# Performance work log

Hardware: AMD Instinct MI355X
Metric: run time of the kernel (lower is better)

Reference implementation:

```python
import jax, jax.numpy as jnp
import numpy as np

B, G, N = 32, 512, 512          # batch, group (POMO rollouts), problem size
EMB, H, DK = 128, 8, 16          # embedding_dim, head_num, qkv_dim (H*DK == EMB)
E, FH, K = 8, 512, 2             # num_experts, ff_hidden_dim, top-k
SQRT_EMB = 11.313708498984761    # sqrt(128), model_params['sqrt_embedding_dim']
CLIP = 10.0                      # logit_clipping


def setup_inputs() -> dict:
    key = jax.random.key(0)
    ks = jax.random.split(key, 22)
    s = 0.05
    d = {}
    d["pref"] = jax.random.uniform(ks[0], (2,), dtype=jnp.float32)
    d["graph"] = jax.random.normal(ks[1], (B, 1, EMB), dtype=jnp.float32)
    d["capacity"] = jax.random.uniform(ks[2], (B, G), dtype=jnp.float32)
    d["encoded_nodes"] = jax.random.normal(ks[3], (B, N, EMB), dtype=jnp.float32)
    d["ninf_mask"] = jnp.zeros((B, G, N), dtype=jnp.float32)
    # hyper-network MLP (note: original has NO activations between hyper_fc layers)
    d["fc1_w"] = jax.random.normal(ks[4], (256, 2)) * s
    d["fc1_b"] = jax.random.normal(ks[5], (256,)) * s
    d["fc2_w"] = jax.random.normal(ks[6], (256, 256)) * s
    d["fc2_b"] = jax.random.normal(ks[7], (256,)) * s
    d["fc3_w"] = jax.random.normal(ks[8], (8, 256)) * s
    d["fc3_b"] = jax.random.normal(ks[9], (8,)) * s
    # hyper heads producing the attention weight matrices (Linear(embd_dim=2, out), no bias)
    d["hWq"] = jax.random.normal(ks[10], ((1 + EMB) * H * DK, 2)) * 0.02
    d["hWk"] = jax.random.normal(ks[11], (EMB * H * DK, 2)) * 0.02
    d["hWv"] = jax.random.normal(ks[12], (EMB * H * DK, 2)) * 0.02
    d["hWc"] = jax.random.normal(ks[13], (EMB * H * DK, 2)) * 0.02
    # MoE combine layer: gating (token input + 8-dim pref embedding) and E expert MLPs
    d["gate_w"] = jax.random.normal(ks[14], (H * DK, E)) * s
    d["gate_pref_w"] = jax.random.normal(ks[15], (8, E)) * s
    d["e_w1"] = jax.random.normal(ks[16], (E, FH, H * DK)) * (1.0 / np.sqrt(H * DK))
    d["e_b1"] = jnp.zeros((E, FH), dtype=jnp.float32)
    d["e_w2"] = jax.random.normal(ks[17], (E, EMB, FH)) * (1.0 / np.sqrt(FH))
    d["e_b2"] = jnp.zeros((E, EMB), dtype=jnp.float32)
    d = {k2: v.astype(jnp.float32) for k2, v in d.items()}
    return d


def _heads(x):  # [B, n, H*DK] -> [B, H, n, DK]
    b, n, _ = x.shape
    return x.reshape(b, n, H, DK).transpose(0, 2, 1, 3)


def reference(pref, graph, capacity, encoded_nodes, ninf_mask,
              fc1_w, fc1_b, fc2_w, fc2_b, fc3_w, fc3_b,
              hWq, hWk, hWv, hWc,
              gate_w, gate_pref_w, e_w1, e_b1, e_w2, e_b2):
    # ---- assign(pref): hypernet generates attention weight matrices ----
    h = fc1_w @ pref + fc1_b
    h = fc2_w @ h + fc2_b
    mid = fc3_w @ h + fc3_b                      # [8] == mid_embd_pref
    Wq = (hWq @ mid[0:2]).reshape(H * DK, 1 + EMB)
    Wk = (hWk @ mid[2:4]).reshape(H * DK, EMB)
    Wv = (hWv @ mid[4:6]).reshape(H * DK, EMB)
    Wc = (hWc @ mid[6:8]).reshape(H * DK, EMB)
    # ---- set_kv ----
    k = _heads(encoded_nodes @ Wk.T)             # [B,H,N,DK]
    v = _heads(encoded_nodes @ Wv.T)
    # ---- forward ----
    inp = jnp.concatenate(
        [jnp.broadcast_to(graph, (B, G, EMB)), capacity[:, :, None]], axis=2)
    q = _heads(inp @ Wq.T)                       # [B,H,G,DK]
    score = jnp.einsum('bhgd,bhnd->bhgn', q, k) / jnp.sqrt(jnp.float32(DK))
    score = score + ninf_mask[:, None, :, :]
    attn = jax.nn.softmax(score, axis=3)
    out = jnp.einsum('bhgn,bhnd->bhgd', attn, v)
    out = out.transpose(0, 2, 1, 3).reshape(B, G, H * DK)   # [B,G,128]
    # ---- MoE combine (noisy top-k gating, deterministic at inference) ----
    logits = out @ gate_w + mid @ gate_pref_w    # [B,G,E]
    vals, idx = jax.lax.top_k(logits, K)
    gv = jax.nn.softmax(vals, axis=-1)           # softmax over selected k (T=1)
    gates = jnp.sum(jax.nn.one_hot(idx, E, dtype=out.dtype) * gv[..., None], axis=-2)
    hdn = jax.nn.relu(jnp.einsum('bgi,ehi->bgeh', out, e_w1) + e_b1)
    y = jnp.einsum('bgeh,eoh->bgeo', hdn, e_w2) + e_b2
    moe_out = jnp.einsum('bgeo,bge->bgo', y, gates)          # [B,G,EMB]
    # ---- combine + tanh-clipped masked softmax over nodes ----
    mh = moe_out @ Wc.T                           # [B,G,EMB]
    sc = jnp.einsum('bge,bne->bgn', mh, encoded_nodes) / SQRT_EMB
    probs = jax.nn.softmax(CLIP * jnp.tanh(sc) + ninf_mask, axis=2)
    return probs
```

## Files before the change

kernel.cpp:

```cpp
#include <hip/hip_runtime.h>


typedef __attribute__((ext_vector_type(8))) __bf16 bf16x8;
typedef __attribute__((ext_vector_type(4))) float f32x4;

static constexpr long OFF_MID   = 0;
static constexpr long OFF_PREFL = 8;
static constexpr long OFF_WQ    = 64;
static constexpr long OFF_WKB   = 16576;
static constexpr long OFF_WVB   = 24768;
static constexpr long OFF_WCB   = 32960;
static constexpr long OFF_QB    = 65728;
static constexpr long OFF_CNT   = 69824;
static constexpr long OFF_TOK   = 69888;
static constexpr long OFF_WGT   = 200960;
static constexpr long OFF_AO    = 332288;
static constexpr long OFF_MH    = 2429440;
static constexpr long OFF_ENCB  = 3478016;

__device__ __forceinline__ unsigned f2bf(float x) {
  union { float f; unsigned u; } v; v.f = x;
  return ((v.u + 0x7FFFu + ((v.u >> 16) & 1u)) >> 16) & 0xFFFFu;
}

__global__ __launch_bounds__(256)
void k_hyper(const float* __restrict__ pref, const float* __restrict__ fc1w,
             const float* __restrict__ fc1b, const float* __restrict__ fc2w,
             const float* __restrict__ fc2b, const float* __restrict__ fc3w,
             const float* __restrict__ fc3b, const float* __restrict__ gpw,
             float* __restrict__ ws) {
  __shared__ float h1[256];
  __shared__ float h2[256];
  __shared__ float mid[8];
  const int t = threadIdx.x;
  const float p0 = pref[0], p1 = pref[1];
  h1[t] = fc1w[2*t]*p0 + fc1w[2*t+1]*p1 + fc1b[t];
  __syncthreads();
  float s = 0.f;
  for (int j = 0; j < 256; ++j) s = fmaf(fc2w[t*256+j], h1[j], s);
  h2[t] = s + fc2b[t];
  __syncthreads();
  if (t < 8) {
    float s2 = 0.f;
    for (int j = 0; j < 256; ++j) s2 = fmaf(fc3w[t*256+j], h2[j], s2);
    mid[t] = s2 + fc3b[t];
    ws[OFF_MID + t] = mid[t];
  }
  __syncthreads();
  if (t < 8) {
    float s3 = 0.f;
    for (int i = 0; i < 8; ++i) s3 = fmaf(mid[i], gpw[i*8 + t], s3);
    ws[OFF_PREFL + t] = s3;
  }
}

__global__ __launch_bounds__(256)
void k_hyperw(const float* __restrict__ hWq, const float* __restrict__ hWk,
              const float* __restrict__ hWv, const float* __restrict__ hWc,
              float* __restrict__ ws) {
  const int i = blockIdx.x*256 + threadIdx.x;
  const float m0 = ws[0], m1 = ws[1], m2 = ws[2], m3 = ws[3],
              m4 = ws[4], m5 = ws[5], m6 = ws[6], m7 = ws[7];
  if (i < 16512) {
    ws[OFF_WQ + i] = hWq[2*i]*m0 + hWq[2*i+1]*m1;
  } else if (i < 32896) {
    const int j = i - 16512;
    ((unsigned short*)(ws + OFF_WKB))[j] = (unsigned short)f2bf(hWk[2*j]*m2 + hWk[2*j+1]*m3);
  } else if (i < 49280) {
    const int j = i - 32896;
    ((unsigned short*)(ws + OFF_WVB))[j] = (unsigned short)f2bf(hWv[2*j]*m4 + hWv[2*j+1]*m5);
  } else if (i < 65664) {
    const int j = i - 49280;
    ((unsigned short*)(ws + OFF_WCB))[j] = (unsigned short)f2bf(hWc[2*j]*m6 + hWc[2*j+1]*m7);
  }
}

__global__ __launch_bounds__(256)
void k_cvt(const float* __restrict__ ew1, const float* __restrict__ ew2,
           const float* __restrict__ enc,
           unsigned short* __restrict__ w1b, unsigned short* __restrict__ w2b,
           unsigned short* __restrict__ encb) {
  const int i = blockIdx.x*256 + threadIdx.x;
  const float* src;
  unsigned short* dst;
  if (i < 131072)      { src = ew1 + (long)i*4;          dst = w1b + (long)i*4; }
  else if (i < 262144) { src = ew2 + (long)(i-131072)*4; dst = w2b + (long)(i-131072)*4; }
  else                 { src = enc + (long)(i-262144)*4; dst = encb + (long)(i-262144)*4; }
  const float4 v = *(const float4*)src;
  uint2 p;
  p.x = f2bf(v.x) | (f2bf(v.y) << 16);
  p.y = f2bf(v.z) | (f2bf(v.w) << 16);
  *(uint2*)dst = p;
}

__global__ __launch_bounds__(128)
void k_qbase(const float* __restrict__ graph, float* __restrict__ ws) {
  __shared__ float g[128];
  const int b = blockIdx.x, t = threadIdx.x;
  g[t] = graph[b*128 + t];
  __syncthreads();
  const float* wq = ws + OFF_WQ + (long)t*129;
  float s = 0.f;
  for (int i = 0; i < 128; ++i) s = fmaf(g[i], wq[i], s);
  ws[OFF_QB + b*128 + t] = s;
}

__device__ __forceinline__ bf16x8 ld_frag(const unsigned short* base, int row, int bytecol) {
  const int addr = row*256 + (bytecol ^ ((row & 7) << 4));
  return *(const bf16x8*)((const char*)base + addr);
}

__global__ __launch_bounds__(256)
void k_kv(const unsigned short* __restrict__ encb,
          const unsigned short* __restrict__ wkb,
          const unsigned short* __restrict__ wvb,
          unsigned short* __restrict__ Kb, unsigned short* __restrict__ Vb) {
  __shared__ unsigned short Ws[128*128];
  __shared__ unsigned short Xs[64*128];
  const int tid = threadIdx.x;
  const int nbase = blockIdx.x * 64;
  const unsigned short* Wb = blockIdx.y ? wvb : wkb;
  unsigned short* Cb = blockIdx.y ? Vb : Kb;
#pragma unroll
  for (int s = 0; s < 8; ++s) {
    const int id = tid + s*256;
    const int fr = id >> 4, c16 = id & 15;
    const uint4 v = *(const uint4*)(Wb + (long)fr*128 + c16*8);
    *(uint4*)((char*)Ws + fr*256 + ((c16*16) ^ ((fr & 7) << 4))) = v;
  }
#pragma unroll
  for (int s = 0; s < 4; ++s) {
    const int id = tid + s*256;
    const int r = id >> 4, c16 = id & 15;
    const uint4 v = *(const uint4*)(encb + (long)(nbase + r)*128 + c16*8);
    *(uint4*)((char*)Xs + r*256 + ((c16*16) ^ ((r & 7) << 4))) = v;
  }
  __syncthreads();
  const int w = tid >> 6, l = tid & 63, lq = l >> 4, lr = l & 15;
  f32x4 acc[2][4];
#pragma unroll
  for (int a = 0; a < 2; ++a)
#pragma unroll
    for (int m = 0; m < 4; ++m) acc[a][m] = (f32x4){0.f, 0.f, 0.f, 0.f};
#pragma unroll
  for (int ks = 0; ks < 4; ++ks) {
    const int bcol = ks*64 + lq*16;
    const bf16x8 a0 = ld_frag(Ws, (2*w  )*16 + lr, bcol);
    const bf16x8 a1 = ld_frag(Ws, (2*w+1)*16 + lr, bcol);
    const bf16x8 b0 = ld_frag(Xs, 0*16 + lr, bcol);
    const bf16x8 b1 = ld_frag(Xs, 1*16 + lr, bcol);
    const bf16x8 b2 = ld_frag(Xs, 2*16 + lr, bcol);
    const bf16x8 b3 = ld_frag(Xs, 3*16 + lr, bcol);
    acc[0][0] = __builtin_amdgcn_mfma_f32_16x16x32_bf16(a0, b0, acc[0][0], 0, 0, 0);
    acc[0][1] = __builtin_amdgcn_mfma_f32_16x16x32_bf16(a0, b1, acc[0][1], 0, 0, 0);
    acc[0][2] = __builtin_amdgcn_mfma_f32_16x16x32_bf16(a0, b2, acc[0][2], 0, 0, 0);
    acc[0][3] = __builtin_amdgcn_mfma_f32_16x16x32_bf16(a0, b3, acc[0][3], 0, 0, 0);
    acc[1][0] = __builtin_amdgcn_mfma_f32_16x16x32_bf16(a1, b0, acc[1][0], 0, 0, 0);
    acc[1][1] = __builtin_amdgcn_mfma_f32_16x16x32_bf16(a1, b1, acc[1][1], 0, 0, 0);
    acc[1][2] = __builtin_amdgcn_mfma_f32_16x16x32_bf16(a1, b2, acc[1][2], 0, 0, 0);
    acc[1][3] = __builtin_amdgcn_mfma_f32_16x16x32_bf16(a1, b3, acc[1][3], 0, 0, 0);
  }
#pragma unroll
  for (int obi = 0; obi < 2; ++obi) {
    const int o0 = (2*w + obi)*16 + lq*4;
#pragma unroll
    for (int mb = 0; mb < 4; ++mb) {
      const long n = nbase + mb*16 + lr;
      uint2 pp;
      pp.x = f2bf(acc[obi][mb][0]) | (f2bf(acc[obi][mb][1]) << 16);
      pp.y = f2bf(acc[obi][mb][2]) | (f2bf(acc[obi][mb][3]) << 16);
      *(uint2*)(Cb + n*128 + o0) = pp;
    }
  }
}

__global__ __launch_bounds__(256)
void k_mh(const float* __restrict__ Y0, const float* __restrict__ Y1,
          const unsigned short* __restrict__ wcb,
          unsigned short* __restrict__ mhb) {
  __shared__ unsigned short Ws[128*128];
  __shared__ unsigned short Xs[64*128];
  const int tid = threadIdx.x;
  const int nbase = blockIdx.x * 64;
#pragma unroll
  for (int s = 0; s < 8; ++s) {
    const int id = tid + s*256;
    const int fr = id >> 4, c16 = id & 15;
    const uint4 v = *(const uint4*)(wcb + (long)fr*128 + c16*8);
    *(uint4*)((char*)Ws + fr*256 + ((c16*16) ^ ((fr & 7) << 4))) = v;
  }
#pragma unroll
  for (int s = 0; s < 4; ++s) {
    const int id = tid + s*256;
    const int r = id >> 4, c16 = id & 15;
    const long base = (long)(nbase + r)*128 + c16*8;
    const float4 a0 = *(const float4*)(Y0 + base);
    const float4 a1 = *(const float4*)(Y0 + base + 4);
    const float4 b0 = *(const float4*)(Y1 + base);
    const float4 b1 = *(const float4*)(Y1 + base + 4);
    uint4 p;
    p.x = f2bf(a0.x + b0.x) | (f2bf(a0.y + b0.y) << 16);
    p.y = f2bf(a0.z + b0.z) | (f2bf(a0.w + b0.w) << 16);
    p.z = f2bf(a1.x + b1.x) | (f2bf(a1.y + b1.y) << 16);
    p.w = f2bf(a1.z + b1.z) | (f2bf(a1.w + b1.w) << 16);
    *(uint4*)((char*)Xs + r*256 + ((c16*16) ^ ((r & 7) << 4))) = p;
  }
  __syncthreads();
  const int w = tid >> 6, l = tid & 63, lq = l >> 4, lr = l & 15;
  f32x4 acc[2][4];
#pragma unroll
  for (int a = 0; a < 2; ++a)
#pragma unroll
    for (int m = 0; m < 4; ++m) acc[a][m] = (f32x4){0.f, 0.f, 0.f, 0.f};
#pragma unroll
  for (int ks = 0; ks < 4; ++ks) {
    const int bcol = ks*64 + lq*16;
    const bf16x8 a0 = ld_frag(Ws, (2*w  )*16 + lr, bcol);
    const bf16x8 a1 = ld_frag(Ws, (2*w+1)*16 + lr, bcol);
    const bf16x8 b0 = ld_frag(Xs, 0*16 + lr, bcol);
    const bf16x8 b1 = ld_frag(Xs, 1*16 + lr, bcol);
    const bf16x8 b2 = ld_frag(Xs, 2*16 + lr, bcol);
    const bf16x8 b3 = ld_frag(Xs, 3*16 + lr, bcol);
    acc[0][0] = __builtin_amdgcn_mfma_f32_16x16x32_bf16(a0, b0, acc[0][0], 0, 0, 0);
    acc[0][1] = __builtin_amdgcn_mfma_f32_16x16x32_bf16(a0, b1, acc[0][1], 0, 0, 0);
    acc[0][2] = __builtin_amdgcn_mfma_f32_16x16x32_bf16(a0, b2, acc[0][2], 0, 0, 0);
    acc[0][3] = __builtin_amdgcn_mfma_f32_16x16x32_bf16(a0, b3, acc[0][3], 0, 0, 0);
    acc[1][0] = __builtin_amdgcn_mfma_f32_16x16x32_bf16(a1, b0, acc[1][0], 0, 0, 0);
    acc[1][1] = __builtin_amdgcn_mfma_f32_16x16x32_bf16(a1, b1, acc[1][1], 0, 0, 0);
    acc[1][2] = __builtin_amdgcn_mfma_f32_16x16x32_bf16(a1, b2, acc[1][2], 0, 0, 0);
    acc[1][3] = __builtin_amdgcn_mfma_f32_16x16x32_bf16(a1, b3, acc[1][3], 0, 0, 0);
  }
#pragma unroll
  for (int obi = 0; obi < 2; ++obi) {
    const int o0 = (2*w + obi)*16 + lq*4;
#pragma unroll
    for (int mb = 0; mb < 4; ++mb) {
      const long n = nbase + mb*16 + lr;
      uint2 pp;
      pp.x = f2bf(acc[obi][mb][0]) | (f2bf(acc[obi][mb][1]) << 16);
      pp.y = f2bf(acc[obi][mb][2]) | (f2bf(acc[obi][mb][3]) << 16);
      *(uint2*)(mhb + n*128 + o0) = pp;
    }
  }
}

__global__ __launch_bounds__(512)
void k_attn(const unsigned short* __restrict__ Kb,
            const unsigned short* __restrict__ Vb,
            const float* __restrict__ ws, const float* __restrict__ cap,
            const float* __restrict__ mask, float* __restrict__ AO) {
  const int bid = blockIdx.x;
  const int b = bid & 31, h = (bid >> 5) & 7, qh = bid >> 8;
  __shared__ unsigned short Kbf[512*24];
  __shared__ unsigned short Vt[16*536];
  __shared__ unsigned short Ps[8*16*136];
  const int tid = threadIdx.x;
#pragma unroll
  for (int it = 0; it < 2; ++it) {
    const int i = tid + it*512;
    const int n = i >> 1, hf = i & 1;
    const long src = (long)(b*512 + n)*128 + h*16 + hf*8;
    const uint4 kv = *(const uint4*)(Kb + src);
    *(uint4*)(Kbf + n*24 + hf*8) = kv;
    const uint4 vv = *(const uint4*)(Vb + src);
    const unsigned short* sp = (const unsigned short*)&vv;
#pragma unroll
    for (int j = 0; j < 8; ++j) Vt[(hf*8 + j)*536 + n] = sp[j];
  }
  const int w = tid >> 6, l = tid & 63;
  const int lq = l >> 4, lr = l & 15;
  float qb8[8], wl8[8];
  if (lq < 2) {
    const float* qbp = ws + OFF_QB + b*128 + h*16 + lq*8;
    const float* wqp = ws + OFF_WQ;
#pragma unroll
    for (int j = 0; j < 8; ++j) {
      qb8[j] = qbp[j];
      wl8[j] = wqp[(h*16 + lq*8 + j)*129 + 128];
    }
  }
  unsigned short* Pw = Ps + w*16*136;
  __syncthreads();
  const float SC = 0.25f;
  for (int qb = 0; qb < 2; ++qb) {
    const int grow = qh*256 + w*32 + qb*16 + lr;
    bf16x8 qf;
    {
      union { uint4 u; bf16x8 v; } cv;
      cv.u = make_uint4(0u, 0u, 0u, 0u);
      if (lq < 2) {
        const float cp = cap[b*512 + grow];
        float qv[8];
#pragma unroll
        for (int j = 0; j < 8; ++j) qv[j] = (qb8[j] + cp*wl8[j]) * SC;
        cv.u.x = f2bf(qv[0]) | (f2bf(qv[1]) << 16);
        cv.u.y = f2bf(qv[2]) | (f2bf(qv[3]) << 16);
        cv.u.z = f2bf(qv[4]) | (f2bf(qv[5]) << 16);
        cv.u.w = f2bf(qv[6]) | (f2bf(qv[7]) << 16);
      }
      qf = cv.v;
    }
    float m = -3.0e38f, lsum = 0.f;
    f32x4 oacc = {0.f, 0.f, 0.f, 0.f};
    const float* mrow = mask + ((long)(b*512 + grow))*512 + lq*4;
    float4 mk[8];
#pragma unroll
    for (int nb = 0; nb < 8; ++nb) mk[nb] = *(const float4*)(mrow + nb*16);
    for (int ch = 0; ch < 4; ++ch) {
      const int n0 = ch*128;
      f32x4 s[8];
#pragma unroll
      for (int nb = 0; nb < 8; ++nb) {
        bf16x8 kf;
        {
          union { uint4 u; bf16x8 v; } cv;
          cv.u = make_uint4(0u, 0u, 0u, 0u);
          if (lq < 2) cv.u = *(const uint4*)(Kbf + (n0 + nb*16 + lr)*24 + lq*8);
          kf = cv.v;
        }
        s[nb] = __builtin_amdgcn_mfma_f32_16x16x32_bf16(
            kf, qf, (f32x4){0.f, 0.f, 0.f, 0.f}, 0, 0, 0);
        s[nb][0] += mk[nb].x; s[nb][1] += mk[nb].y;
        s[nb][2] += mk[nb].z; s[nb][3] += mk[nb].w;
      }
      if (ch < 3) {
#pragma unroll
        for (int nb = 0; nb < 8; ++nb)
          mk[nb] = *(const float4*)(mrow + (ch+1)*128 + nb*16);
      }
      f32x4 mx = s[0];
#pragma unroll
      for (int nb = 1; nb < 8; ++nb) {
        mx[0] = fmaxf(mx[0], s[nb][0]); mx[1] = fmaxf(mx[1], s[nb][1]);
        mx[2] = fmaxf(mx[2], s[nb][2]); mx[3] = fmaxf(mx[3], s[nb][3]);
      }
      float cm = fmaxf(fmaxf(mx[0], mx[1]), fmaxf(mx[2], mx[3]));
      cm = fmaxf(cm, __shfl_xor(cm, 16));
      cm = fmaxf(cm, __shfl_xor(cm, 32));
      const float nm = fmaxf(m, cm);
      const float rs = __expf(m - nm);
      lsum *= rs;
      oacc[0] *= rs; oacc[1] *= rs; oacc[2] *= rs; oacc[3] *= rs;
      m = nm;
      float ls = 0.f;
#pragma unroll
      for (int nb = 0; nb < 8; ++nb) {
        const float p0 = __expf(s[nb][0] - m);
        const float p1 = __expf(s[nb][1] - m);
        const float p2 = __expf(s[nb][2] - m);
        const float p3 = __expf(s[nb][3] - m);
        ls += (p0 + p1) + (p2 + p3);
        uint2 pp;
        asm("v_cvt_pk_bf16_f32 %0, %1, %2" : "=v"(pp.x) : "v"(p0), "v"(p1));
        asm("v_cvt_pk_bf16_f32 %0, %1, %2" : "=v"(pp.y) : "v"(p2), "v"(p3));
        *(uint2*)(Pw + lr*136 + nb*16 + lq*4) = pp;
      }
      lsum += ls;
#pragma unroll
      for (int ks = 0; ks < 4; ++ks) {
        const bf16x8 va = *(const bf16x8*)(Vt + lr*536 + n0 + ks*32 + lq*8);
        const bf16x8 pb = *(const bf16x8*)(Pw + lr*136 + ks*32 + lq*8);
        oacc = __builtin_amdgcn_mfma_f32_16x16x32_bf16(va, pb, oacc, 0, 0, 0);
      }
    }
    lsum += __shfl_xor(lsum, 16);
    lsum += __shfl_xor(lsum, 32);
    const float inv = 1.f / lsum;
    float4 o;
    o.x = oacc[0]*inv; o.y = oacc[1]*inv; o.z = oacc[2]*inv; o.w = oacc[3]*inv;
    *(float4*)(AO + (long)(b*512 + grow)*128 + h*16 + lq*4) = o;
  }
}

__global__ __launch_bounds__(256)
void k_gate(const float* __restrict__ AO, const float* __restrict__ gw,
            float* __restrict__ ws) {
  const int tid = threadIdx.x;
  const int t = blockIdx.x*256 + tid;
  const float* x = AO + (long)t*128;
  float lg[8];
  {
    const float* pl = ws + OFF_PREFL;
#pragma unroll
    for (int e = 0; e < 8; ++e) lg[e] = pl[e];
  }
  for (int i = 0; i < 128; i += 4) {
    const float4 xv = *(const float4*)(x + i);
#pragma unroll
    for (int u = 0; u < 4; ++u) {
      const float xi = (&xv.x)[u];
      const float4 ga = *(const float4*)(gw + (i+u)*8);
      const float4 gb = *(const float4*)(gw + (i+u)*8 + 4);
      lg[0] = fmaf(xi, ga.x, lg[0]); lg[1] = fmaf(xi, ga.y, lg[1]);
      lg[2] = fmaf(xi, ga.z, lg[2]); lg[3] = fmaf(xi, ga.w, lg[3]);
      lg[4] = fmaf(xi, gb.x, lg[4]); lg[5] = fmaf(xi, gb.y, lg[5]);
      lg[6] = fmaf(xi, gb.z, lg[6]); lg[7] = fmaf(xi, gb.w, lg[7]);
    }
  }
  int i0 = 0; float v0 = lg[0];
#pragma unroll
  for (int e = 1; e < 8; ++e) if (lg[e] > v0) { v0 = lg[e]; i0 = e; }
  int i1 = -1; float v1 = -1e30f;
#pragma unroll
  for (int e = 0; e < 8; ++e) if (e != i0 && lg[e] > v1) { v1 = lg[e]; i1 = e; }
  const float e1 = __expf(v1 - v0);
  const float w0 = 1.f / (1.f + e1);
  const float w1 = 1.f - w0;
  __shared__ int bcnt[8];
  __shared__ int gbase[8];
  if (tid < 8) bcnt[tid] = 0;
  __syncthreads();
  const int p0 = atomicAdd(&bcnt[i0], 1);
  const int p1 = atomicAdd(&bcnt[i1], 1);
  __syncthreads();
  if (tid < 8) {
    int* cnt = (int*)(ws + OFF_CNT);
    gbase[tid] = (bcnt[tid] > 0) ? atomicAdd(&cnt[tid], bcnt[tid]) : 0;
  }
  __syncthreads();
  int* tokp = (int*)(ws + OFF_TOK);
  float* wgtp = ws + OFF_WGT;
  const int s0 = gbase[i0] + p0;
  tokp[i0*16384 + s0] = t;
  wgtp[i0*16384 + s0] = w0;
  const int s1 = gbase[i1] + p1;
  tokp[i1*16384 + s1] = t | (1 << 30);
  wgtp[i1*16384 + s1] = w1;
}

__global__ __launch_bounds__(256)
void k_moe(const float* __restrict__ AO,
           const unsigned short* __restrict__ w1b,
           const unsigned short* __restrict__ w2b,
           const float* __restrict__ eb1, const float* __restrict__ eb2,
           float* __restrict__ ws,
           float* __restrict__ Y0, float* __restrict__ Y1) {
  const int e = blockIdx.y;
  const int ce = ((const int*)(ws + OFF_CNT))[e];
  const int base = blockIdx.x * 64;
  if (base >= ce) return;
  const int nt = min(64, ce - base);

  __shared__ unsigned short Xs[64*128];
  __shared__ unsigned short Wts[128*128];
  __shared__ unsigned short Hs[64*128];
  __shared__ float seb1[512];
  __shared__ float seb2[128];
  __shared__ int   stok[64];
  __shared__ float swgt[64];

  const int tid = threadIdx.x;
  if (tid < 64) {
    if (tid < nt) {
      stok[tid] = ((const int*)(ws + OFF_TOK))[e*16384 + base + tid];
      swgt[tid] = (ws + OFF_WGT)[e*16384 + base + tid];
    } else { stok[tid] = -1; swgt[tid] = 0.f; }
  }
  for (int i = tid; i < 512; i += 256) seb1[i] = eb1[e*512 + i];
  if (tid < 128) seb2[tid] = eb2[e*128 + tid];
  __syncthreads();

#pragma unroll
  for (int r8 = 0; r8 < 8; ++r8) {
    const int id = tid + r8*256;
    const int r = id >> 5, c = id & 31;
    const int pk = stok[r];
    float4 xv = make_float4(0.f, 0.f, 0.f, 0.f);
    if (pk >= 0) xv = *(const float4*)(AO + (long)(pk & 0x3FFFFFFF)*128 + c*4);
    uint2 pkd;
    pkd.x = f2bf(xv.x) | (f2bf(xv.y) << 16);
    pkd.y = f2bf(xv.z) | (f2bf(xv.w) << 16);
    const int bc = (c*8) ^ ((r & 7) << 4);
    *(uint2*)((char*)Xs + r*256 + bc) = pkd;
  }

  const int w  = tid >> 6;
  const int l  = tid & 63;
  const int lq = l >> 4;
  const int lr = l & 15;

  f32x4 yacc[2][4];
#pragma unroll
  for (int a = 0; a < 2; ++a)
#pragma unroll
    for (int m = 0; m < 4; ++m) yacc[a][m] = (f32x4){0.f, 0.f, 0.f, 0.f};

  for (int fc = 0; fc < 4; ++fc) {
    __syncthreads();
    {
      const long wb = (long)(e*512 + fc*128) * 128;
#pragma unroll
      for (int s = 0; s < 8; ++s) {
        const int id = tid + s*256;
        const int fr = id >> 4, c16 = id & 15;
        const uint4 v = *(const uint4*)(w1b + wb + (long)fr*128 + c16*8);
        *(uint4*)((char*)Wts + fr*256 + ((c16*16) ^ ((fr & 7) << 4))) = v;
      }
    }
    __syncthreads();
    f32x4 hacc[2][4];
#pragma unroll
    for (int a = 0; a < 2; ++a)
#pragma unroll
      for (int m = 0; m < 4; ++m) hacc[a][m] = (f32x4){0.f, 0.f, 0.f, 0.f};
#pragma unroll
    for (int ks = 0; ks < 4; ++ks) {
      const int bcol = ks*64 + lq*16;
      const bf16x8 a0 = ld_frag(Wts, (2*w  )*16 + lr, bcol);
      const bf16x8 a1 = ld_frag(Wts, (2*w+1)*16 + lr, bcol);
      const bf16x8 b0 = ld_frag(Xs,  0*16 + lr, bcol);
      const bf16x8 b1 = ld_frag(Xs,  1*16 + lr, bcol);
      const bf16x8 b2 = ld_frag(Xs,  2*16 + lr, bcol);
      const bf16x8 b3 = ld_frag(Xs,  3*16 + lr, bcol);
      hacc[0][0] = __builtin_amdgcn_mfma_f32_16x16x32_bf16(a0, b0, hacc[0][0], 0, 0, 0);
      hacc[0][1] = __builtin_amdgcn_mfma_f32_16x16x32_bf16(a0, b1, hacc[0][1], 0, 0, 0);
      hacc[0][2] = __builtin_amdgcn_mfma_f32_16x16x32_bf16(a0, b2, hacc[0][2], 0, 0, 0);
      hacc[0][3] = __builtin_amdgcn_mfma_f32_16x16x32_bf16(a0, b3, hacc[0][3], 0, 0, 0);
      hacc[1][0] = __builtin_amdgcn_mfma_f32_16x16x32_bf16(a1, b0, hacc[1][0], 0, 0, 0);
      hacc[1][1] = __builtin_amdgcn_mfma_f32_16x16x32_bf16(a1, b1, hacc[1][1], 0, 0, 0);
      hacc[1][2] = __builtin_amdgcn_mfma_f32_16x16x32_bf16(a1, b2, hacc[1][2], 0, 0, 0);
      hacc[1][3] = __builtin_amdgcn_mfma_f32_16x16x32_bf16(a1, b3, hacc[1][3], 0, 0, 0);
    }
    __syncthreads();
#pragma unroll
    for (int fbi = 0; fbi < 2; ++fbi) {
      const int fb = (2*w + fbi)*16 + lq*4;
      const float4 bia = *(const float4*)&seb1[fc*128 + fb];
#pragma unroll
      for (int mb = 0; mb < 4; ++mb) {
        const int m = mb*16 + lr;
        const float h0 = fmaxf(hacc[fbi][mb][0] + bia.x, 0.f);
        const float h1 = fmaxf(hacc[fbi][mb][1] + bia.y, 0.f);
        const float h2 = fmaxf(hacc[fbi][mb][2] + bia.z, 0.f);
        const float h3 = fmaxf(hacc[fbi][mb][3] + bia.w, 0.f);
        uint2 p;
        p.x = f2bf(h0) | (f2bf(h1) << 16);
        p.y = f2bf(h2) | (f2bf(h3) << 16);
        const int bc = (fb*2) ^ ((m & 7) << 4);
        *(uint2*)((char*)Hs + m*256 + bc) = p;
      }
    }
    {
      const long wb = (long)(e*128) * 512 + fc*128;
#pragma unroll
      for (int s = 0; s < 8; ++s) {
        const int id = tid + s*256;
        const int orr = id >> 4, c16 = id & 15;
        const uint4 v = *(const uint4*)(w2b + wb + (long)orr*512 + c16*8);
        *(uint4*)((char*)Wts + orr*256 + ((c16*16) ^ ((orr & 7) << 4))) = v;
      }
    }
    __syncthreads();
#pragma unroll
    for (int ks = 0; ks < 4; ++ks) {
      const int bcol = ks*64 + lq*16;
      const bf16x8 a0 = ld_frag(Wts, (2*w  )*16 + lr, bcol);
      const bf16x8 a1 = ld_frag(Wts, (2*w+1)*16 + lr, bcol);
      const bf16x8 b0 = ld_frag(Hs,  0*16 + lr, bcol);
      const bf16x8 b1 = ld_frag(Hs,  1*16 + lr, bcol);
      const bf16x8 b2 = ld_frag(Hs,  2*16 + lr, bcol);
      const bf16x8 b3 = ld_frag(Hs,  3*16 + lr, bcol);
      yacc[0][0] = __builtin_amdgcn_mfma_f32_16x16x32_bf16(a0, b0, yacc[0][0], 0, 0, 0);
      yacc[0][1] = __builtin_amdgcn_mfma_f32_16x16x32_bf16(a0, b1, yacc[0][1], 0, 0, 0);
      yacc[0][2] = __builtin_amdgcn_mfma_f32_16x16x32_bf16(a0, b2, yacc[0][2], 0, 0, 0);
      yacc[0][3] = __builtin_amdgcn_mfma_f32_16x16x32_bf16(a0, b3, yacc[0][3], 0, 0, 0);
      yacc[1][0] = __builtin_amdgcn_mfma_f32_16x16x32_bf16(a1, b0, yacc[1][0], 0, 0, 0);
      yacc[1][1] = __builtin_amdgcn_mfma_f32_16x16x32_bf16(a1, b1, yacc[1][1], 0, 0, 0);
      yacc[1][2] = __builtin_amdgcn_mfma_f32_16x16x32_bf16(a1, b2, yacc[1][2], 0, 0, 0);
      yacc[1][3] = __builtin_amdgcn_mfma_f32_16x16x32_bf16(a1, b3, yacc[1][3], 0, 0, 0);
    }
  }
#pragma unroll
  for (int obi = 0; obi < 2; ++obi) {
    const int ob = (2*w + obi)*16 + lq*4;
    const float4 b2 = *(const float4*)&seb2[ob];
#pragma unroll
    for (int mb = 0; mb < 4; ++mb) {
      const int tl = mb*16 + lr;
      if (tl < nt) {
        const int pk = stok[tl];
        const int tk = pk & 0x3FFFFFFF;
        const float wgt = swgt[tl];
        float* Yp = ((pk >> 30) ? Y1 : Y0) + (long)tk*128 + ob;
        float4 o;
        o.x = (yacc[obi][mb][0] + b2.x) * wgt;
        o.y = (yacc[obi][mb][1] + b2.y) * wgt;
        o.z = (yacc[obi][mb][2] + b2.z) * wgt;
        o.w = (yacc[obi][mb][3] + b2.w) * wgt;
        *(float4*)Yp = o;
      }
    }
  }
}

__global__ __launch_bounds__(512)
void k_gemm2f(const unsigned short* __restrict__ mhb,
              const unsigned short* __restrict__ encb,
              const float* __restrict__ mask,
              float* __restrict__ out) {
  const int bid = blockIdx.x;
  const int b = bid & 31, rt = bid >> 5;
  __shared__ unsigned short Amh[64*128];
  __shared__ unsigned short Bch[512*32];
  __shared__ float red[64][9];
  const int tid = threadIdx.x;
  const int w = tid >> 6, l = tid & 63, lq = l >> 4, lr = l & 15;
  const long rowbase = (long)b*512 + rt*64;
#pragma unroll
  for (int s = 0; s < 2; ++s) {
    const int id = tid + s*512;
    const int r = id >> 4, c16 = id & 15;
    const uint4 v = *(const uint4*)(mhb + (rowbase + r)*128 + c16*8);
    *(uint4*)((char*)Amh + r*256 + ((c16*16) ^ ((r & 7) << 4))) = v;
  }
  f32x4 acc[4][4];
#pragma unroll
  for (int mi = 0; mi < 4; ++mi)
#pragma unroll
    for (int ni = 0; ni < 4; ++ni) acc[mi][ni] = (f32x4){0.f, 0.f, 0.f, 0.f};
  for (int kc = 0; kc < 4; ++kc) {
    __syncthreads();
#pragma unroll
    for (int s = 0; s < 4; ++s) {
      const int id = tid + s*512;
      const int n = id >> 2, sl = id & 3;
      const uint4 v = *(const uint4*)(encb + ((long)b*512 + n)*128 + kc*32 + sl*8);
      *(uint4*)((char*)Bch + n*64 + ((sl*16) ^ ((n & 3) << 4))) = v;
    }
    __syncthreads();
    bf16x8 af[4], bfr[4];
#pragma unroll
    for (int mi = 0; mi < 4; ++mi) {
      const int r = mi*16 + lr;
      af[mi] = *(const bf16x8*)((const char*)Amh + r*256 + ((kc*64 + lq*16) ^ ((r & 7) << 4)));
    }
#pragma unroll
    for (int ni = 0; ni < 4; ++ni) {
      const int n = w*64 + ni*16 + lr;
      bfr[ni] = *(const bf16x8*)((const char*)Bch + n*64 + ((lq*16) ^ ((n & 3) << 4)));
    }
#pragma unroll
    for (int mi = 0; mi < 4; ++mi)
#pragma unroll
      for (int ni = 0; ni < 4; ++ni)
        acc[mi][ni] = __builtin_amdgcn_mfma_f32_16x16x32_bf16(af[mi], bfr[ni], acc[mi][ni], 0, 0, 0);
  }
  const float ISC = 1.f/11.313708498984761f;
  float rsum[4][4];
#pragma unroll
  for (int mi = 0; mi < 4; ++mi)
#pragma unroll
    for (int j = 0; j < 4; ++j) rsum[mi][j] = 0.f;
#pragma unroll
  for (int mi = 0; mi < 4; ++mi) {
#pragma unroll
    for (int j = 0; j < 4; ++j) {
      const long row = rowbase + mi*16 + lq*4 + j;
      const float* mrow = mask + row*512 + w*64 + lr;
#pragma unroll
      for (int ni = 0; ni < 4; ++ni) {
        const float sc = acc[mi][ni][j] * ISC;
        const float li = 10.f*tanhf(sc) + mrow[ni*16];
        const float e = __expf(li - 10.f);
        acc[mi][ni][j] = e;
        rsum[mi][j] += e;
      }
    }
  }
#pragma unroll
  for (int mi = 0; mi < 4; ++mi)
#pragma unroll
    for (int j = 0; j < 4; ++j) {
#pragma unroll
      for (int o = 1; o < 16; o <<= 1) rsum[mi][j] += __shfl_xor(rsum[mi][j], o);
    }
  if (lr == 0) {
#pragma unroll
    for (int mi = 0; mi < 4; ++mi)
#pragma unroll
      for (int j = 0; j < 4; ++j) red[mi*16 + lq*4 + j][w] = rsum[mi][j];
  }
  __syncthreads();
  if (tid < 64) {
    float s = 0.f;
#pragma unroll
    for (int wv = 0; wv < 8; ++wv) s += red[tid][wv];
    red[tid][8] = 1.f / s;
  }
  __syncthreads();
#pragma unroll
  for (int mi = 0; mi < 4; ++mi) {
#pragma unroll
    for (int j = 0; j < 4; ++j) {
      const int rl = mi*16 + lq*4 + j;
      const float inv = red[rl][8];
      float* orow = out + (rowbase + rl)*512 + w*64 + lr;
#pragma unroll
      for (int ni = 0; ni < 4; ++ni) orow[ni*16] = acc[mi][ni][j] * inv;
    }
  }
}

extern "C" void kernel_launch(void* const* d_in, const int* in_sizes, int n_in,
                              void* d_out, int out_size, void* d_ws, size_t ws_size,
                              hipStream_t stream) {
  (void)in_sizes; (void)n_in; (void)out_size; (void)ws_size;
  const float* pref  = (const float*)d_in[0];
  const float* graph = (const float*)d_in[1];
  const float* cap   = (const float*)d_in[2];
  const float* enc   = (const float*)d_in[3];
  const float* mask  = (const float*)d_in[4];
  const float* fc1w  = (const float*)d_in[5];
  const float* fc1b  = (const float*)d_in[6];
  const float* fc2w  = (const float*)d_in[7];
  const float* fc2b  = (const float*)d_in[8];
  const float* fc3w  = (const float*)d_in[9];
  const float* fc3b  = (const float*)d_in[10];
  const float* hWq   = (const float*)d_in[11];
  const float* hWk   = (const float*)d_in[12];
  const float* hWv   = (const float*)d_in[13];
  const float* hWc   = (const float*)d_in[14];
  const float* gw    = (const float*)d_in[15];
  const float* gpw   = (const float*)d_in[16];
  const float* ew1   = (const float*)d_in[17];
  const float* eb1   = (const float*)d_in[18];
  const float* ew2   = (const float*)d_in[19];
  const float* eb2   = (const float*)d_in[20];
  float* ws  = (float*)d_ws;
  float* out = (float*)d_out;
  unsigned short* Kbuf = (unsigned short*)out;
  unsigned short* Vbuf = (unsigned short*)(out + 1048576);
  float* Y0 = out;
  float* Y1 = out + 2097152;
  unsigned short* ew1b = (unsigned short*)(out + 4194304);
  unsigned short* ew2b = (unsigned short*)(out + 4456448);
  unsigned short* mhb  = (unsigned short*)(ws + OFF_MH);
  unsigned short* encb = (unsigned short*)(ws + OFF_ENCB);
  unsigned short* wkb  = (unsigned short*)(ws + OFF_WKB);
  unsigned short* wvb  = (unsigned short*)(ws + OFF_WVB);
  unsigned short* wcb  = (unsigned short*)(ws + OFF_WCB);

  hipMemsetAsync((char*)d_ws + OFF_CNT*sizeof(float), 0, 8*sizeof(int), stream);
  k_cvt<<<3072, 256, 0, stream>>>(ew1, ew2, enc, ew1b, ew2b, encb);
  k_hyper<<<1, 256, 0, stream>>>(pref, fc1w, fc1b, fc2w, fc2b, fc3w, fc3b, gpw, ws);
  k_hyperw<<<257, 256, 0, stream>>>(hWq, hWk, hWv, hWc, ws);
  k_qbase<<<32, 128, 0, stream>>>(graph, ws);
  k_kv<<<dim3(256, 2), 256, 0, stream>>>(encb, wkb, wvb, Kbuf, Vbuf);
  k_attn<<<512, 512, 0, stream>>>(Kbuf, Vbuf, ws, cap, mask, ws + OFF_AO);
  k_gate<<<64, 256, 0, stream>>>(ws + OFF_AO, gw, ws);
  k_moe<<<dim3(256, 8), 256, 0, stream>>>(ws + OFF_AO, ew1b, ew2b, eb1, eb2, ws, Y0, Y1);
  k_mh<<<256, 256, 0, stream>>>(Y0, Y1, wcb, mhb);
  k_gemm2f<<<256, 512, 0, stream>>>(mhb, encb, mask, out);
}
```

Measured before the change: 132.6 us.

## Fuse prep kernels into one launch and retile attention for more blocks

Merges the bf16 conversion, hyper-network MLP, hyper weight generation, q-base projection and counter reset into a single k_prep launch, recomputing the small MLP per block to avoid serial kernel dependencies. Restructures the attention kernel to 1024 blocks with 16 query rows per wave and 32-key chunks, replacing padded LDS layouts with XOR swizzles and setting occupancy bounds. Trades redundant MLP compute and more online-softmax rescale steps for fewer launches and higher parallelism and occupancy.

```diff
diff --git a/kernel.cpp b/kernel.cpp
--- a/kernel.cpp
+++ b/kernel.cpp
@@ -6,17 +6,17 @@
 
 static constexpr long OFF_MID   = 0;
 static constexpr long OFF_PREFL = 8;
-static constexpr long OFF_WQ    = 64;
-static constexpr long OFF_WKB   = 16576;
-static constexpr long OFF_WVB   = 24768;
-static constexpr long OFF_WCB   = 32960;
-static constexpr long OFF_QB    = 65728;
-static constexpr long OFF_CNT   = 69824;
-static constexpr long OFF_TOK   = 69888;
-static constexpr long OFF_WGT   = 200960;
-static constexpr long OFF_AO    = 332288;
-static constexpr long OFF_MH    = 2429440;
-static constexpr long OFF_ENCB  = 3478016;
+static constexpr long OFF_WL    = 16;
+static constexpr long OFF_WKB   = 256;
+static constexpr long OFF_WVB   = 8448;
+static constexpr long OFF_WCB   = 16640;
+static constexpr long OFF_QB    = 24832;
+static constexpr long OFF_CNT   = 28928;
+static constexpr long OFF_TOK   = 28936;
+static constexpr long OFF_WGT   = 160008;
+static constexpr long OFF_AO    = 291080;
+static constexpr long OFF_MH    = 2388232;
+static constexpr long OFF_ENCB  = 3436808;
 
 __device__ __forceinline__ unsigned f2bf(float x) {
   union { float f; unsigned u; } v; v.f = x;
@@ -24,85 +24,97 @@
 }
 
 __global__ __launch_bounds__(256)
-void k_hyper(const float* __restrict__ pref, const float* __restrict__ fc1w,
-             const float* __restrict__ fc1b, const float* __restrict__ fc2w,
-             const float* __restrict__ fc2b, const float* __restrict__ fc3w,
-             const float* __restrict__ fc3b, const float* __restrict__ gpw,
-             float* __restrict__ ws) {
+void k_prep(const float* __restrict__ pref, const float* __restrict__ fc1w,
+            const float* __restrict__ fc1b, const float* __restrict__ fc2w,
+            const float* __restrict__ fc2b, const float* __restrict__ fc3w,
+            const float* __restrict__ fc3b, const float* __restrict__ gpw,
+            const float* __restrict__ graph,
+            const float* __restrict__ hWq, const float* __restrict__ hWk,
+            const float* __restrict__ hWv, const float* __restrict__ hWc,
+            const float* __restrict__ ew1, const float* __restrict__ ew2,
+            const float* __restrict__ enc,
+            unsigned short* __restrict__ w1b, unsigned short* __restrict__ w2b,
+            unsigned short* __restrict__ encb, float* __restrict__ ws) {
+  const int bid = blockIdx.x;
+  const int tid = threadIdx.x;
+  if (bid < 3072) {
+    const int i = bid*256 + tid;
+    const float* src;
+    unsigned short* dst;
+    if (i < 131072)      { src = ew1 + (long)i*4;          dst = w1b + (long)i*4; }
+    else if (i < 262144) { src = ew2 + (long)(i-131072)*4; dst = w2b + (long)(i-131072)*4; }
+    else                 { src = enc + (long)(i-262144)*4; dst = encb + (long)(i-262144)*4; }
+    const float4 v = *(const float4*)src;
+    uint2 p;
+    p.x = f2bf(v.x) | (f2bf(v.y) << 16);
+    p.y = f2bf(v.z) | (f2bf(v.w) << 16);
+    *(uint2*)dst = p;
+    return;
+  }
   __shared__ float h1[256];
   __shared__ float h2[256];
   __shared__ float mid[8];
-  const int t = threadIdx.x;
+  __shared__ float g[2][128];
   const float p0 = pref[0], p1 = pref[1];
-  h1[t] = fc1w[2*t]*p0 + fc1w[2*t+1]*p1 + fc1b[t];
+  h1[tid] = fc1w[2*tid]*p0 + fc1w[2*tid+1]*p1 + fc1b[tid];
   __syncthreads();
   float s = 0.f;
-  for (int j = 0; j < 256; ++j) s = fmaf(fc2w[t*256+j], h1[j], s);
-  h2[t] = s + fc2b[t];
-  __syncthreads();
-  if (t < 8) {
+  for (int j = 0; j < 256; ++j) s = fmaf(fc2w[tid*256+j], h1[j], s);
+  h2[tid] = s + fc2b[tid];
+  __syncthreads();
+  if (tid < 8) {
     float s2 = 0.f;
-    for (int j = 0; j < 256; ++j) s2 = fmaf(fc3w[t*256+j], h2[j], s2);
-    mid[t] = s2 + fc3b[t];
-    ws[OFF_MID + t] = mid[t];
-  }
-  __syncthreads();
-  if (t < 8) {
-    float s3 = 0.f;
-    for (int i = 0; i < 8; ++i) s3 = fmaf(mid[i], gpw[i*8 + t], s3);
-    ws[OFF_PREFL + t] = s3;
-  }
-}
-
-__global__ __launch_bounds__(256)
-void k_hyperw(const float* __restrict__ hWq, const float* __restrict__ hWk,
-              const float* __restrict__ hWv, const float* __restrict__ hWc,
-              float* __restrict__ ws) {
-  const int i = blockIdx.x*256 + threadIdx.x;
-  const float m0 = ws[0], m1 = ws[1], m2 = ws[2], m3 = ws[3],
-              m4 = ws[4], m5 = ws[5], m6 = ws[6], m7 = ws[7];
-  if (i < 16512) {
-    ws[OFF_WQ + i] = hWq[2*i]*m0 + hWq[2*i+1]*m1;
-  } else if (i < 32896) {
-    const int j = i - 16512;
-    ((unsigned short*)(ws + OFF_WKB))[j] = (unsigned short)f2bf(hWk[2*j]*m2 + hWk[2*j+1]*m3);
-  } else if (i < 49280) {
-    const int j = i - 32896;
-    ((unsigned short*)(ws + OFF_WVB))[j] = (unsigned short)f2bf(hWv[2*j]*m4 + hWv[2*j+1]*m5);
-  } else if (i < 65664) {
-    const int j = i - 49280;
-    ((unsigned short*)(ws + OFF_WCB))[j] = (unsigned short)f2bf(hWc[2*j]*m6 + hWc[2*j+1]*m7);
-  }
-}
-
-__global__ __launch_bounds__(256)
-void k_cvt(const float* __restrict__ ew1, const float* __restrict__ ew2,
-           const float* __restrict__ enc,
-           unsigned short* __restrict__ w1b, unsigned short* __restrict__ w2b,
-           unsigned short* __restrict__ encb) {
-  const int i = blockIdx.x*256 + threadIdx.x;
-  const float* src;
-  unsigned short* dst;
-  if (i < 131072)      { src = ew1 + (long)i*4;          dst = w1b + (long)i*4; }
-  else if (i < 262144) { src = ew2 + (long)(i-131072)*4; dst = w2b + (long)(i-131072)*4; }
-  else                 { src = enc + (long)(i-262144)*4; dst = encb + (long)(i-262144)*4; }
-  const float4 v = *(const float4*)src;
-  uint2 p;
-  p.x = f2bf(v.x) | (f2bf(v.y) << 16);
-  p.y = f2bf(v.z) | (f2bf(v.w) << 16);
-  *(uint2*)dst = p;
-}
-
-__global__ __launch_bounds__(128)
-void k_qbase(const float* __restrict__ graph, float* __restrict__ ws) {
-  __shared__ float g[128];
-  const int b = blockIdx.x, t = threadIdx.x;
-  g[t] = graph[b*128 + t];
-  __syncthreads();
-  const float* wq = ws + OFF_WQ + (long)t*129;
-  float s = 0.f;
-  for (int i = 0; i < 128; ++i) s = fmaf(g[i], wq[i], s);
-  ws[OFF_QB + b*128 + t] = s;
+    for (int j = 0; j < 256; ++j) s2 = fmaf(fc3w[tid*256+j], h2[j], s2);
+    mid[tid] = s2 + fc3b[tid];
+  }
+  __syncthreads();
+  if (bid < 3264) {
+    const int i = (bid - 3072)*256 + tid;
+    if (i < 16384) {
+      ((unsigned short*)(ws + OFF_WKB))[i] =
+          (unsigned short)f2bf(hWk[2*i]*mid[2] + hWk[2*i+1]*mid[3]);
+    } else if (i < 32768) {
+      const int j = i - 16384;
+      ((unsigned short*)(ws + OFF_WVB))[j] =
+          (unsigned short)f2bf(hWv[2*j]*mid[4] + hWv[2*j+1]*mid[5]);
+    } else {
+      const int j = i - 32768;
+      ((unsigned short*)(ws + OFF_WCB))[j] =
+          (unsigned short)f2bf(hWc[2*j]*mid[6] + hWc[2*j+1]*mid[7]);
+    }
+    return;
+  }
+  const int qb = bid - 3264;
+  const int b0 = qb*2;
+  {
+    const int bb = tid >> 7, ii = tid & 127;
+    g[bb][ii] = graph[(b0+bb)*128 + ii];
+  }
+  __syncthreads();
+  const float m0 = mid[0], m1 = mid[1];
+  {
+    const int bb = tid >> 7, o = tid & 127;
+    const float* hq = hWq + (long)o*129*2;
+    float acc = 0.f;
+    for (int i2 = 0; i2 < 128; ++i2) {
+      const float w = hq[2*i2]*m0 + hq[2*i2+1]*m1;
+      acc = fmaf(g[bb][i2], w, acc);
+    }
+    ws[OFF_QB + (b0+bb)*128 + o] = acc;
+  }
+  if (qb == 0) {
+    if (tid < 8) {
+      ws[OFF_MID + tid] = mid[tid];
+      float s3 = 0.f;
+      for (int i2 = 0; i2 < 8; ++i2) s3 = fmaf(mid[i2], gpw[i2*8 + tid], s3);
+      ws[OFF_PREFL + tid] = s3;
+      ((int*)(ws + OFF_CNT))[tid] = 0;
+    }
+    if (tid >= 16 && tid < 144) {
+      const int o = tid - 16;
+      ws[OFF_WL + o] = hWq[((long)o*129 + 128)*2]*m0 + hWq[((long)o*129 + 128)*2 + 1]*m1;
+    }
+  }
 }
 
 __device__ __forceinline__ bf16x8 ld_frag(const unsigned short* base, int row, int bytecol) {
@@ -244,16 +256,16 @@
   }
 }
 
-__global__ __launch_bounds__(512)
+__global__ __launch_bounds__(512, 8)
 void k_attn(const unsigned short* __restrict__ Kb,
             const unsigned short* __restrict__ Vb,
             const float* __restrict__ ws, const float* __restrict__ cap,
             const float* __restrict__ mask, float* __restrict__ AO) {
   const int bid = blockIdx.x;
   const int b = bid & 31, h = (bid >> 5) & 7, qh = bid >> 8;
-  __shared__ unsigned short Kbf[512*24];
-  __shared__ unsigned short Vt[16*536];
-  __shared__ unsigned short Ps[8*16*136];
+  __shared__ unsigned short Kbf[512*16];
+  __shared__ unsigned short Vt[16*512];
+  __shared__ unsigned short Ps[8*16*32];
   const int tid = threadIdx.x;
 #pragma unroll
   for (int it = 0; it < 2; ++it) {
@@ -261,115 +273,94 @@
     const int n = i >> 1, hf = i & 1;
     const long src = (long)(b*512 + n)*128 + h*16 + hf*8;
     const uint4 kv = *(const uint4*)(Kb + src);
-    *(uint4*)(Kbf + n*24 + hf*8) = kv;
+    *(uint4*)(Kbf + n*16 + hf*8) = kv;
     const uint4 vv = *(const uint4*)(Vb + src);
     const unsigned short* sp = (const unsigned short*)&vv;
 #pragma unroll
-    for (int j = 0; j < 8; ++j) Vt[(hf*8 + j)*536 + n] = sp[j];
+    for (int j = 0; j < 8; ++j) {
+      const int d = hf*8 + j;
+      Vt[d*512 + (n ^ ((d & 7) << 3))] = sp[j];
+    }
   }
   const int w = tid >> 6, l = tid & 63;
   const int lq = l >> 4, lr = l & 15;
-  float qb8[8], wl8[8];
-  if (lq < 2) {
-    const float* qbp = ws + OFF_QB + b*128 + h*16 + lq*8;
-    const float* wqp = ws + OFF_WQ;
-#pragma unroll
-    for (int j = 0; j < 8; ++j) {
-      qb8[j] = qbp[j];
-      wl8[j] = wqp[(h*16 + lq*8 + j)*129 + 128];
-    }
-  }
-  unsigned short* Pw = Ps + w*16*136;
-  __syncthreads();
-  const float SC = 0.25f;
-  for (int qb = 0; qb < 2; ++qb) {
-    const int grow = qh*256 + w*32 + qb*16 + lr;
-    bf16x8 qf;
-    {
-      union { uint4 u; bf16x8 v; } cv;
-      cv.u = make_uint4(0u, 0u, 0u, 0u);
-      if (lq < 2) {
-        const float cp = cap[b*512 + grow];
-        float qv[8];
-#pragma unroll
-        for (int j = 0; j < 8; ++j) qv[j] = (qb8[j] + cp*wl8[j]) * SC;
-        cv.u.x = f2bf(qv[0]) | (f2bf(qv[1]) << 16);
-        cv.u.y = f2bf(qv[2]) | (f2bf(qv[3]) << 16);
-        cv.u.z = f2bf(qv[4]) | (f2bf(qv[5]) << 16);
-        cv.u.w = f2bf(qv[6]) | (f2bf(qv[7]) << 16);
+  const int grow = qh*128 + w*16 + lr;
+  bf16x8 qf;
+  {
+    union { uint4 u; bf16x8 v; } cv;
+    cv.u = make_uint4(0u, 0u, 0u, 0u);
+    if (lq < 2) {
+      const float* qbp = ws + OFF_QB + b*128 + h*16 + lq*8;
+      const float* wlp = ws + OFF_WL + h*16 + lq*8;
+      const float cp = cap[b*512 + grow];
+      float qv[8];
+#pragma unroll
+      for (int j = 0; j < 8; ++j) qv[j] = (qbp[j] + cp*wlp[j]) * 0.25f;
+      cv.u.x = f2bf(qv[0]) | (f2bf(qv[1]) << 16);
+      cv.u.y = f2bf(qv[2]) | (f2bf(qv[3]) << 16);
+      cv.u.z = f2bf(qv[4]) | (f2bf(qv[5]) << 16);
+      cv.u.w = f2bf(qv[6]) | (f2bf(qv[7]) << 16);
+    }
+    qf = cv.v;
+  }
+  unsigned short* Pw = Ps + w*16*32;
+  const int psw = (lr & 3) << 3;
+  __syncthreads();
+  float m = -3.0e38f, lsum = 0.f;
+  f32x4 oacc = {0.f, 0.f, 0.f, 0.f};
+  const float* mrow = mask + ((long)(b*512 + grow))*512 + lq*4;
+  for (int qc = 0; qc < 16; ++qc) {
+    const int n0 = qc*32;
+    f32x4 s[2];
+#pragma unroll
+    for (int nb = 0; nb < 2; ++nb) {
+      bf16x8 kf;
+      {
+        union { uint4 u; bf16x8 v; } cv;
+        cv.u = make_uint4(0u, 0u, 0u, 0u);
+        if (lq < 2) cv.u = *(const uint4*)(Kbf + (n0 + nb*16 + lr)*16 + lq*8);
+        kf = cv.v;
       }
-      qf = cv.v;
-    }
-    float m = -3.0e38f, lsum = 0.f;
-    f32x4 oacc = {0.f, 0.f, 0.f, 0.f};
-    const float* mrow = mask + ((long)(b*512 + grow))*512 + lq*4;
-    float4 mk[8];
-#pragma unroll
-    for (int nb = 0; nb < 8; ++nb) mk[nb] = *(const float4*)(mrow + nb*16);
-    for (int ch = 0; ch < 4; ++ch) {
-      const int n0 = ch*128;
-      f32x4 s[8];
-#pragma unroll
-      for (int nb = 0; nb < 8; ++nb) {
-        bf16x8 kf;
-        {
-          union { uint4 u; bf16x8 v; } cv;
-          cv.u = make_uint4(0u, 0u, 0u, 0u);
-          if (lq < 2) cv.u = *(const uint4*)(Kbf + (n0 + nb*16 + lr)*24 + lq*8);
-          kf = cv.v;
-        }
-        s[nb] = __builtin_amdgcn_mfma_f32_16x16x32_bf16(
-            kf, qf, (f32x4){0.f, 0.f, 0.f, 0.f}, 0, 0, 0);
-        s[nb][0] += mk[nb].x; s[nb][1] += mk[nb].y;
-        s[nb][2] += mk[nb].z; s[nb][3] += mk[nb].w;
-      }
-      if (ch < 3) {
-#pragma unroll
-        for (int nb = 0; nb < 8; ++nb)
-          mk[nb] = *(const float4*)(mrow + (ch+1)*128 + nb*16);
-      }
-      f32x4 mx = s[0];
-#pragma unroll
-      for (int nb = 1; nb < 8; ++nb) {
-        mx[0] = fmaxf(mx[0], s[nb][0]); mx[1] = fmaxf(mx[1], s[nb][1]);
-        mx[2] = fmaxf(mx[2], s[nb][2]); mx[3] = fmaxf(mx[3], s[nb][3]);
-      }
-      float cm = fmaxf(fmaxf(mx[0], mx[1]), fmaxf(mx[2], mx[3]));
-      cm = fmaxf(cm, __shfl_xor(cm, 16));
-      cm = fmaxf(cm, __shfl_xor(cm, 32));
-      const float nm = fmaxf(m, cm);
-      const float rs = __expf(m - nm);
-      lsum *= rs;
-      oacc[0] *= rs; oacc[1] *= rs; oacc[2] *= rs; oacc[3] *= rs;
-      m = nm;
-      float ls = 0.f;
-#pragma unroll
-      for (int nb = 0; nb < 8; ++nb) {
-        const float p0 = __expf(s[nb][0] - m);
-        const float p1 = __expf(s[nb][1] - m);
-        const float p2 = __expf(s[nb][2] - m);
-        const float p3 = __expf(s[nb][3] - m);
-        ls += (p0 + p1) + (p2 + p3);
-        uint2 pp;
-        asm("v_cvt_pk_bf16_f32 %0, %1, %2" : "=v"(pp.x) : "v"(p0), "v"(p1));
-        asm("v_cvt_pk_bf16_f32 %0, %1, %2" : "=v"(pp.y) : "v"(p2), "v"(p3));
-        *(uint2*)(Pw + lr*136 + nb*16 + lq*4) = pp;
-      }
-      lsum += ls;
-#pragma unroll
-      for (int ks = 0; ks < 4; ++ks) {
-        const bf16x8 va = *(const bf16x8*)(Vt + lr*536 + n0 + ks*32 + lq*8);
-        const bf16x8 pb = *(const bf16x8*)(Pw + lr*136 + ks*32 + lq*8);
-        oacc = __builtin_amdgcn_mfma_f32_16x16x32_bf16(va, pb, oacc, 0, 0, 0);
-      }
-    }
-    lsum += __shfl_xor(lsum, 16);
-    lsum += __shfl_xor(lsum, 32);
-    const float inv = 1.f / lsum;
-    float4 o;
-    o.x = oacc[0]*inv; o.y = oacc[1]*inv; o.z = oacc[2]*inv; o.w = oacc[3]*inv;
-    *(float4*)(AO + (long)(b*512 + grow)*128 + h*16 + lq*4) = o;
-  }
+      s[nb] = __builtin_amdgcn_mfma_f32_16x16x32_bf16(
+          kf, qf, (f32x4){0.f, 0.f, 0.f, 0.f}, 0, 0, 0);
+      const float4 mk = *(const float4*)(mrow + n0 + nb*16);
+      s[nb][0] += mk.x; s[nb][1] += mk.y; s[nb][2] += mk.z; s[nb][3] += mk.w;
+    }
+    f32x4 mx;
+    mx[0] = fmaxf(s[0][0], s[1][0]); mx[1] = fmaxf(s[0][1], s[1][1]);
+    mx[2] = fmaxf(s[0][2], s[1][2]); mx[3] = fmaxf(s[0][3], s[1][3]);
+    float cm = fmaxf(fmaxf(mx[0], mx[1]), fmaxf(mx[2], mx[3]));
+    cm = fmaxf(cm, __shfl_xor(cm, 16));
+    cm = fmaxf(cm, __shfl_xor(cm, 32));
+    const float nm = fmaxf(m, cm);
+    const float rs = __expf(m - nm);
+    lsum *= rs;
+    oacc[0] *= rs; oacc[1] *= rs; oacc[2] *= rs; oacc[3] *= rs;
+    m = nm;
+    float ls = 0.f;
+#pragma unroll
+    for (int nb = 0; nb < 2; ++nb) {
+      const float e0 = __expf(s[nb][0] - m);
+      const float e1 = __expf(s[nb][1] - m);
+      const float e2 = __expf(s[nb][2] - m);
+      const float e3 = __expf(s[nb][3] - m);
+      ls += (e0 + e1) + (e2 + e3);
+      uint2 pp;
+      asm("v_cvt_pk_bf16_f32 %0, %1, %2" : "=v"(pp.x) : "v"(e0), "v"(e1));
+      asm("v_cvt_pk_bf16_f32 %0, %1, %2" : "=v"(pp.y) : "v"(e2), "v"(e3));
+      *(uint2*)(Pw + lr*32 + ((nb*16 + lq*4) ^ psw)) = pp;
+    }
+    lsum += ls;
+    const bf16x8 va = *(const bf16x8*)(Vt + lr*512 + ((n0 + lq*8) ^ ((lr & 7) << 3)));
+    const bf16x8 pb = *(const bf16x8*)(Pw + lr*32 + ((lq*8) ^ psw));
+    oacc = __builtin_amdgcn_mfma_f32_16x16x32_bf16(va, pb, oacc, 0, 0, 0);
+  }
+  lsum += __shfl_xor(lsum, 16);
+  lsum += __shfl_xor(lsum, 32);
+  const float inv = 1.f / lsum;
+  float4 o;
+  o.x = oacc[0]*inv; o.y = oacc[1]*inv; o.z = oacc[2]*inv; o.w = oacc[3]*inv;
+  *(float4*)(AO + (long)(b*512 + grow)*128 + h*16 + lq*4) = o;
 }
 
 __global__ __launch_bounds__(256)
@@ -740,13 +731,11 @@
   unsigned short* wvb  = (unsigned short*)(ws + OFF_WVB);
   unsigned short* wcb  = (unsigned short*)(ws + OFF_WCB);
 
-  hipMemsetAsync((char*)d_ws + OFF_CNT*sizeof(float), 0, 8*sizeof(int), stream);
-  k_cvt<<<3072, 256, 0, stream>>>(ew1, ew2, enc, ew1b, ew2b, encb);
-  k_hyper<<<1, 256, 0, stream>>>(pref, fc1w, fc1b, fc2w, fc2b, fc3w, fc3b, gpw, ws);
-  k_hyperw<<<257, 256, 0, stream>>>(hWq, hWk, hWv, hWc, ws);
-  k_qbase<<<32, 128, 0, stream>>>(graph, ws);
+  k_prep<<<3280, 256, 0, stream>>>(pref, fc1w, fc1b, fc2w, fc2b, fc3w, fc3b,
+                                   gpw, graph, hWq, hWk, hWv, hWc,
+                                   ew1, ew2, enc, ew1b, ew2b, encb, ws);
   k_kv<<<dim3(256, 2), 256, 0, stream>>>(encb, wkb, wvb, Kbuf, Vbuf);
-  k_attn<<<512, 512, 0, stream>>>(Kbuf, Vbuf, ws, cap, mask, ws + OFF_AO);
+  k_attn<<<1024, 512, 0, stream>>>(Kbuf, Vbuf, ws, cap, mask, ws + OFF_AO);
   k_gate<<<64, 256, 0, stream>>>(ws + OFF_AO, gw, ws);
   k_moe<<<dim3(256, 8), 256, 0, stream>>>(ws + OFF_AO, ew1b, ew2b, eb1, eb2, ws, Y0, Y1);
   k_mh<<<256, 256, 0, stream>>>(Y0, Y1, wcb, mhb);
```

Result: faster. 127.7 us (-3.7%).
